# Kernel optimization log

Hardware: AMD Instinct MI355X
Metric: run time of the kernel (lower is better)

## Reference

```python
import jax, jax.numpy as jnp
import numpy as np

B, T, C = 4, 2048, 2048
H, HD = 16, 128  # n_heads, head_dim; C == H*HD


def _rope_rotate(x, cos, sin):
    """x: [b,t,h,d]; cos/sin: [t, d//2]. Complex multiply on interleaved pairs,
    matching torch view_as_complex on reshape(..., -1, 2)."""
    xr = x[..., 0::2]  # real parts  [b,t,h,d/2]
    xi = x[..., 1::2]  # imag parts
    c = cos[None, :, None, :]
    s = sin[None, :, None, :]
    or_ = xr * c - xi * s
    oi_ = xr * s + xi * c
    # interleave back: [..., d/2, 2] -> [..., d]
    return jnp.stack([or_, oi_], axis=-1).reshape(x.shape)


def setup_inputs() -> dict:
    key = jax.random.key(0)
    ks = jax.random.split(key, 6)
    x = jax.random.normal(ks[0], (B, T, C), dtype=jnp.float32)
    # causal boolean mask: True = attend
    attn_mask = jnp.tril(jnp.ones((T, T), dtype=bool))
    # standard RoPE frequencies (theta=10000)
    inv_freq = 1.0 / (10000.0 ** (np.arange(0, HD, 2, dtype=np.float32) / HD))
    ang = np.arange(T, dtype=np.float32)[:, None] * inv_freq[None, :]  # [T, HD/2]
    rope_cos = jnp.asarray(np.cos(ang))
    rope_sin = jnp.asarray(np.sin(ang))
    sc = 1.0 / np.sqrt(C)
    Wq = jax.random.normal(ks[1], (C, C), dtype=jnp.float32) * sc
    Wk = jax.random.normal(ks[2], (C, C), dtype=jnp.float32) * sc
    Wv = jax.random.normal(ks[3], (C, C), dtype=jnp.float32) * sc
    Wp = jax.random.normal(ks[4], (C, C), dtype=jnp.float32) * sc
    return {"x": x, "attn_mask": attn_mask, "rope_cos": rope_cos,
            "rope_sin": rope_sin, "Wq": Wq, "Wk": Wk, "Wv": Wv, "Wp": Wp}


def reference(x, attn_mask, rope_cos, rope_sin, Wq, Wk, Wv, Wp):
    b, t, c = x.shape
    # QKV projections (nn.Linear: y = x @ W.T), reshape to heads
    q = jnp.einsum('btc,dc->btd', x, Wq).reshape(b, t, H, HD)
    k = jnp.einsum('btc,dc->btd', x, Wk).reshape(b, t, H, HD)
    v = jnp.einsum('btc,dc->btd', x, Wv).reshape(b, t, H, HD)
    # RoPE on q, k
    q = _rope_rotate(q, rope_cos[:t], rope_sin[:t])
    k = _rope_rotate(k, rope_cos[:t], rope_sin[:t])
    # SDPA with boolean mask, scale 1/sqrt(head_dim)
    scores = jnp.einsum('bqhd,bkhd->bhqk', q, k) / jnp.sqrt(jnp.asarray(HD, x.dtype))
    neg = jnp.finfo(scores.dtype).min
    scores = jnp.where(attn_mask[None, None, :t, :t], scores, neg)
    attn = jax.nn.softmax(scores, axis=-1)
    out = jnp.einsum('bhqk,bkhd->bqhd', attn, v).reshape(b, t, H * HD)
    return jnp.einsum('btd,cd->btc', out, Wp)
```

## Files before the change

### kernel.cpp

```cpp
#include <hip/hip_runtime.h>

#define B_    4
#define T_    2048
#define C_    2048
#define H_    16
#define HD_   128
#define LDQK  4096

typedef __attribute__((ext_vector_type(8))) short short8v;
typedef __attribute__((ext_vector_type(4))) float float4v;
typedef __attribute__((ext_vector_type(16))) float float16v;

typedef const __attribute__((address_space(1))) void* gld_src_t;
typedef __attribute__((address_space(3))) void* gld_dst_t;
#define GLDS16(g, l) __builtin_amdgcn_global_load_lds((gld_src_t)(g), (gld_dst_t)(l), 16, 0, 0)

__device__ __forceinline__ unsigned short f2bf(float f) {
  unsigned int u = __float_as_uint(f);
  u += 0x7fffu + ((u >> 16) & 1u);
  return (unsigned short)(u >> 16);
}
__device__ __forceinline__ float bf2f(unsigned short s) {
  return __uint_as_float(((unsigned int)s) << 16);
}
__device__ __forceinline__ unsigned int cvtpk_bf16(float lo, float hi) {
  unsigned int r;
  asm("v_cvt_pk_bf16_f32 %0, %1, %2" : "=v"(r) : "v"(lo), "v"(hi));
  return r;
}

__global__ void cvt5_kernel(const float* __restrict__ x,
                            const float* __restrict__ wq, const float* __restrict__ wk,
                            const float* __restrict__ wv, const float* __restrict__ wp,
                            unsigned short* __restrict__ xbf, unsigned short* __restrict__ wdst) {
  int i = blockIdx.x * blockDim.x + threadIdx.x;
  const float4* s;
  ushort4* d;
  if (i < 4194304) {
    s = reinterpret_cast<const float4*>(x) + i;
    d = reinterpret_cast<ushort4*>(xbf) + i;
  } else {
    int j = i - 4194304;
    int w = j >> 20;
    const float* wsrc = (w == 0) ? wq : (w == 1) ? wk : (w == 2) ? wv : wp;
    s = reinterpret_cast<const float4*>(wsrc) + (j & 1048575);
    d = reinterpret_cast<ushort4*>(wdst) + j;
  }
  float4 v = *s;
  ushort4 o;
  o.x = f2bf(v.x); o.y = f2bf(v.y); o.z = f2bf(v.z); o.w = f2bf(v.w);
  *d = o;
}


#define ISSUE_HALF(MAT, HA, KT, CBUF)                                             \
  { const unsigned short* gp_ = (MAT) ? Bm : A;                                   \
    const size_t gb_ = (MAT) ? bbase : abase;                                     \
    _Pragma("unroll")                                                             \
    for (int i_ = 0; i_ < 2; ++i_) {                                              \
      int fo_ = (i_ * 512 + tid) * 16;                              \
      int rl_ = fo_ >> 7;                                            \
      int row_ = (HA) * 128 + rl_;                                                \
      int g_ = (fo_ >> 4) & 7;                                                    \
      int ce_ = ((g_ ^ (rl_ & 7)) << 3);              \
      GLDS16(gp_ + gb_ + (size_t)row_ * K + (KT) * 64 + ce_,                      \
             lds + (CBUF) * 65536 + (MAT) * 32768 + (HA) * 16384 + fo_);          \
    } }

#define RD_A(dst, MI, KK, CBUF)                                                   \
  { int row_ = wm * 128 + (MI) * 16 + lr;                                         \
    dst = *reinterpret_cast<const short8v*>(                                      \
        lds + (CBUF) * 65536 + row_ * 128 + (((KK) * 64 + lg * 16) ^ ((row_ & 7) << 4))); }

#define RD_B(dst, NI, KK, CBUF)                                                   \
  { int row_ = wn * 64 + (NI) * 16 + lr;                                          \
    dst = *reinterpret_cast<const short8v*>(                                      \
        lds + (CBUF) * 65536 + 32768 + row_ * 128 + (((KK) * 64 + lg * 16) ^ ((row_ & 7) << 4))); }

#define MFMA16(MB, AV, BV)                                                        \
    _Pragma("unroll")                                                             \
    for (int ni_ = 0; ni_ < 4; ++ni_) {                                           \
      _Pragma("unroll")                                                           \
      for (int mi_ = 0; mi_ < 4; ++mi_)                                           \
        acc[(MB)+mi_][ni_] = __builtin_amdgcn_mfma_f32_16x16x32_bf16(AV[mi_], BV[ni_], acc[(MB)+mi_][ni_], 0,0,0); \
    }

template<int MODE>
__global__ __launch_bounds__(512, 2)
void gemm256(const unsigned short* __restrict__ A, const unsigned short* __restrict__ Bm,
             void* __restrict__ Cout, unsigned short* __restrict__ vtp,
             int K, int NB, int ldc,
             const float* __restrict__ rc, const float* __restrict__ rs)
{
  extern __shared__ char lds[];
  const int tid = threadIdx.x;
  const int l = tid & 63, w = tid >> 6;
  const int lr = l & 15, lg = l >> 4;
  const int wm = w >> 2, wn = w & 3;

  const int nwg = (int)gridDim.x;
  const int orig = (int)blockIdx.x;
  const int qq = nwg >> 3, rr = nwg & 7;
  const int xcd = orig & 7, idx = orig >> 3;
  const int wg = (xcd < rr ? xcd * (qq + 1) : rr * (qq + 1) + (xcd - rr) * qq) + idx;
  const int bm = wg / NB, bn = wg % NB;

  const size_t abase = (size_t)bm * 256 * (size_t)K;
  const size_t bbase = (size_t)bn * 256 * (size_t)K;

  float4v acc[8][4];
  const float4v fz = {0.f, 0.f, 0.f, 0.f};
#pragma unroll
  for (int i = 0; i < 8; ++i)
#pragma unroll
    for (int j = 0; j < 4; ++j) acc[i][j] = fz;

  const int nk = K >> 6;

  ISSUE_HALF(1, 0, 0, 0)
  ISSUE_HALF(1, 1, 0, 0)
  ISSUE_HALF(0, 0, 0, 0)
  ISSUE_HALF(0, 1, 0, 0)
  asm volatile("s_waitcnt vmcnt(0)" ::: "memory");
  __builtin_amdgcn_s_barrier();

  short8v aC[4], aN[4], bC[4], bN[4];
  RD_A(aC[0], 0, 0, 0) RD_A(aC[1], 1, 0, 0) RD_A(aC[2], 2, 0, 0) RD_A(aC[3], 3, 0, 0)
  RD_B(bC[0], 0, 0, 0) RD_B(bC[1], 1, 0, 0) RD_B(bC[2], 2, 0, 0) RD_B(bC[3], 3, 0, 0)

  for (int t = 0; t < nk; ++t) {
    const int c = t & 1;

    if (t + 1 < nk) {
      ISSUE_HALF(1, 0, t + 1, c ^ 1)
      ISSUE_HALF(1, 1, t + 1, c ^ 1)
      ISSUE_HALF(0, 0, t + 1, c ^ 1)
      ISSUE_HALF(0, 1, t + 1, c ^ 1)
    }

    RD_A(aN[0], 4, 0, c) RD_A(aN[1], 5, 0, c) RD_A(aN[2], 6, 0, c) RD_A(aN[3], 7, 0, c)
    MFMA16(0, aC, bC)

    RD_A(aC[0], 0, 1, c) RD_A(aC[1], 1, 1, c) RD_A(aC[2], 2, 1, c) RD_A(aC[3], 3, 1, c)
    RD_B(bN[0], 0, 1, c) RD_B(bN[1], 1, 1, c) RD_B(bN[2], 2, 1, c) RD_B(bN[3], 3, 1, c)
    MFMA16(4, aN, bC)

    RD_A(aN[0], 4, 1, c) RD_A(aN[1], 5, 1, c) RD_A(aN[2], 6, 1, c) RD_A(aN[3], 7, 1, c)
    MFMA16(0, aC, bN)

    asm volatile("s_waitcnt lgkmcnt(0)" ::: "memory");
    __builtin_amdgcn_sched_barrier(0);
    asm volatile("s_waitcnt vmcnt(0)" ::: "memory");
    __builtin_amdgcn_s_barrier();

    MFMA16(4, aN, bN)

    if (t + 1 < nk) {
      RD_A(aC[0], 0, 0, c ^ 1) RD_A(aC[1], 1, 0, c ^ 1) RD_A(aC[2], 2, 0, c ^ 1) RD_A(aC[3], 3, 0, c ^ 1)
      RD_B(bC[0], 0, 0, c ^ 1) RD_B(bC[1], 1, 0, c ^ 1) RD_B(bC[2], 2, 0, c ^ 1) RD_B(bC[3], 3, 0, c ^ 1)
    }
  }

  const int row0 = bm * 256 + wm * 128;
  const int col0 = bn * 256 + wn * 64;
  if (MODE == 3 && bn >= 16) {
#pragma unroll
    for (int mi = 0; mi < 8; ++mi)
#pragma unroll
      for (int ni = 0; ni < 4; ++ni) {
        int vcol = col0 - 4096 + ni * 16 + lr;
        int hh = vcol >> 7, dd = vcol & 127;
        int row = row0 + mi * 16 + lg * 4;
        int bb = row >> 11, t0 = row & 2047;
        ushort4 o4;
        o4.x = f2bf(acc[mi][ni][0]); o4.y = f2bf(acc[mi][ni][1]);
        o4.z = f2bf(acc[mi][ni][2]); o4.w = f2bf(acc[mi][ni][3]);
        *reinterpret_cast<ushort4*>(vtp + (((size_t)(bb * 16 + hh)) << 18) + (((size_t)dd) << 11) + t0) = o4;
      }
  } else if (MODE == 3) {
    const float sgn = (lr & 1) ? 1.0f : -1.0f;
#pragma unroll
    for (int mi = 0; mi < 8; ++mi)
#pragma unroll
      for (int ni = 0; ni < 4; ++ni) {
        int col = col0 + ni * 16 + lr;
        int ii = (col & 127) >> 1;
#pragma unroll
        for (int r2 = 0; r2 < 4; ++r2) {
          int row = row0 + mi * 16 + lg * 4 + r2;
          int tt = row & 2047;
          float v = acc[mi][ni][r2];
          float vp = __shfl_xor(v, 1);
          float cs = rc[tt * 64 + ii];
          float sn = rs[tt * 64 + ii];
          float o = v * cs + sgn * vp * sn;
          ((unsigned short*)Cout)[(size_t)row * ldc + col] = f2bf(o);
        }
      }
  } else {
#pragma unroll
    for (int mi = 0; mi < 8; ++mi)
#pragma unroll
      for (int ni = 0; ni < 4; ++ni)
#pragma unroll
        for (int r2 = 0; r2 < 4; ++r2) {
          int row = row0 + mi * 16 + lg * 4 + r2;
          int col = col0 + ni * 16 + lr;
          ((float*)Cout)[(size_t)row * ldc + col] = acc[mi][ni][r2];
        }
  }
}

__global__ __launch_bounds__(256, 2)
void attn_kernel(const unsigned short* __restrict__ qk,
                 const unsigned short* __restrict__ vt,
                 unsigned short* __restrict__ out)
{
  __shared__ unsigned short Kl[2][64 * 128];
  __shared__ unsigned short Vl[2][128 * 64];

  const int wg = (int)blockIdx.x;
  const int bh = ((wg >> 6) << 3) | (wg & 7);
  const int bx = (wg >> 3) & 7;
  const int b = bh >> 4, h = bh & 15;
  const int tid = threadIdx.x, w = tid >> 6, l = tid & 63;
  const int q32 = l & 31, hi = l >> 5;
  const size_t rowbase = (size_t)b * T_;
  const unsigned short* kbase = qk + rowbase * LDQK + 2048 + h * HD_;
  const unsigned short* vbase = vt + (size_t)bh * (HD_ * (size_t)T_);
  const float SC = 0.12754089f;
  const float16v z16 = {0.f,0.f,0.f,0.f,0.f,0.f,0.f,0.f,0.f,0.f,0.f,0.f,0.f,0.f,0.f,0.f};

#define STAGE(kv0_, bi_)                                                          \
  {                                                                               \
    _Pragma("unroll")                                                             \
    for (int i_ = 0; i_ < 4; ++i_) {                                              \
      int fo = (i_ * 256 + tid) * 16;                                             \
      int row = fo >> 8;                                                          \
      int cb = (fo & 255) ^ ((row & 15) << 4);                                    \
      GLDS16(kbase + (size_t)((kv0_) + row) * LDQK + (cb >> 1), (char*)Kl[bi_] + fo); \
    }                                                                             \
    _Pragma("unroll")                                                             \
    for (int i_ = 0; i_ < 4; ++i_) {                                              \
      int fo = (i_ * 256 + tid) * 16;                                             \
      int r6 = (fo >> 8) & 63;                                                    \
      int s_ = (fo >> 7) & 1;                                                     \
      int dd = r6 | ((s_ ^ ((r6 >> 3) & 1)) << 6);                                \
      int k16 = ((fo >> 4) & 7) ^ (dd & 7);                                       \
      GLDS16(vbase + (size_t)dd * T_ + (kv0_) + k16 * 8, (char*)Vl[bi_] + fo);    \
    }                                                                             \
  }

  for (int sel = 0; sel < 2; ++sel) {
    const int qt = sel ? bx : (15 - bx);
    const int q0w = qt * 128 + w * 32;
    const int qg = q0w + q32;

    short8v qf[8];
#pragma unroll
    for (int kf = 0; kf < 8; ++kf) {
      short8v t = *reinterpret_cast<const short8v*>(
          qk + (rowbase + q0w + q32) * (size_t)LDQK + h * HD_ + kf * 16 + hi * 8);
      short8v r;
#pragma unroll
      for (int e = 0; e < 8; ++e) r[e] = (short)f2bf(bf2f((unsigned short)t[e]) * SC);
      qf[kf] = r;
    }

    float16v o[4];
#pragma unroll
    for (int db = 0; db < 4; ++db) o[db] = z16;
    float m_run = -1e30f, lsum = 0.f;

    const int nkv = 2 * (qt + 1);

    STAGE(0, 0);
    __syncthreads();

    for (int tile = 0; tile < nkv; ++tile) {
      const int kv0 = tile * 64;
      const int bi = tile & 1;
      if (tile + 1 < nkv) STAGE((tile + 1) * 64, bi ^ 1);

      if (kv0 <= q0w + 31) {
        float16v stv[2];
        stv[0] = z16; stv[1] = z16;
        __builtin_amdgcn_s_setprio(1);
#pragma unroll
        for (int kb = 0; kb < 2; ++kb) {
          int key = kb * 32 + q32;
          int swz = (key & 15) << 4;
          int rbase = key * 256;
#pragma unroll
          for (int kf = 0; kf < 8; ++kf) {
            short8v ak = *reinterpret_cast<const short8v*>(
                (char*)Kl[bi] + rbase + ((kf * 32 + hi * 16) ^ swz));
            stv[kb] = __builtin_amdgcn_mfma_f32_32x32x16_bf16(ak, qf[kf], stv[kb], 0, 0, 0);
          }
        }
        __builtin_amdgcn_s_setprio(0);
        if (kv0 + 63 > q0w) {
#pragma unroll
          for (int kb = 0; kb < 2; ++kb)
#pragma unroll
            for (int r = 0; r < 16; ++r) {
              int key = kv0 + kb * 32 + (r & 3) + 8 * ((r >> 2) & 3) + 4 * hi;
              if (key > qg) stv[kb][r] = -1e30f;
            }
        }
        float t16[16];
#pragma unroll
        for (int r = 0; r < 16; ++r) t16[r] = fmaxf(stv[0][r], stv[1][r]);
#pragma unroll
        for (int s = 8; s >= 1; s >>= 1)
#pragma unroll
          for (int r = 0; r < s; ++r) t16[r] = fmaxf(t16[r], t16[r + s]);
        float pm = fmaxf(t16[0], __shfl_xor(t16[0], 32));

        if (!__all(pm <= m_run + 8.0f)) {
          float mn = fmaxf(m_run, pm);
          float fac = exp2f(m_run - mn);
          lsum *= fac;
          m_run = mn;
#pragma unroll
          for (int r = 0; r < 16; ++r) {
            int src = (r & 3) + 8 * ((r >> 2) & 3) + 4 * hi;
            float fr = __shfl(fac, src);
#pragma unroll
            for (int db = 0; db < 4; ++db) o[db][r] *= fr;
          }
        }
        {
          float s16[16];
#pragma unroll
          for (int r = 0; r < 16; ++r) {
            float p0 = exp2f(stv[0][r] - m_run);
            float p1 = exp2f(stv[1][r] - m_run);
            stv[0][r] = p0; stv[1][r] = p1;
            s16[r] = p0 + p1;
          }
#pragma unroll
          for (int s = 8; s >= 1; s >>= 1)
#pragma unroll
            for (int r = 0; r < s; ++r) s16[r] += s16[r + s];
          lsum += s16[0] + __shfl_xor(s16[0], 32);
        }
        unsigned int pw0[8], pw1[8], xw0[8], xw1[8];
#pragma unroll
        for (int j = 0; j < 8; ++j) {
          pw0[j] = cvtpk_bf16(stv[0][2 * j], stv[0][2 * j + 1]);
          pw1[j] = cvtpk_bf16(stv[1][2 * j], stv[1][2 * j + 1]);
        }
#pragma unroll
        for (int j = 0; j < 8; ++j) {
          xw0[j] = __shfl_xor(pw0[j], 32);
          xw1[j] = __shfl_xor(pw1[j], 32);
        }
        union UW { unsigned int u[4]; short8v v; };
        short8v pb[4];
        {
          UW a0, a1, c0, c1;
          a0.u[0] = hi ? xw0[2] : pw0[0];  a0.u[1] = hi ? xw0[3] : pw0[1];
          a0.u[2] = hi ? pw0[2] : xw0[0];  a0.u[3] = hi ? pw0[3] : xw0[1];
          a1.u[0] = hi ? xw0[6] : pw0[4];  a1.u[1] = hi ? xw0[7] : pw0[5];
          a1.u[2] = hi ? pw0[6] : xw0[4];  a1.u[3] = hi ? pw0[7] : xw0[5];
          c0.u[0] = hi ? xw1[2] : pw1[0];  c0.u[1] = hi ? xw1[3] : pw1[1];
          c0.u[2] = hi ? pw1[2] : xw1[0];  c0.u[3] = hi ? pw1[3] : xw1[1];
          c1.u[0] = hi ? xw1[6] : pw1[4];  c1.u[1] = hi ? xw1[7] : pw1[5];
          c1.u[2] = hi ? pw1[6] : xw1[4];  c1.u[3] = hi ? pw1[7] : xw1[5];
          pb[0] = a0.v; pb[1] = a1.v; pb[2] = c0.v; pb[3] = c1.v;
        }
        __builtin_amdgcn_s_setprio(1);
#pragma unroll
        for (int db = 0; db < 4; ++db) {
          int dd = db * 32 + q32;
          int rb2 = (dd & 63) * 256 + ((((dd >> 6) ^ ((dd >> 3) & 1)) & 1) << 7);
          int swz = (dd & 7) << 4;
#pragma unroll
          for (int kb16 = 0; kb16 < 4; ++kb16) {
            short8v bv = *reinterpret_cast<const short8v*>(
                (char*)Vl[bi] + rb2 + ((kb16 * 32 + hi * 16) ^ swz));
            o[db] = __builtin_amdgcn_mfma_f32_32x32x16_bf16(pb[kb16], bv, o[db], 0, 0, 0);
          }
        }
        __builtin_amdgcn_s_setprio(0);
      }
      __syncthreads();
    }

    float linv = 1.0f / lsum;
#pragma unroll
    for (int r = 0; r < 16; ++r) {
      int src = (r & 3) + 8 * ((r >> 2) & 3) + 4 * hi;
      float lr_ = __shfl(linv, src);
      size_t rowoff = (rowbase + q0w + src) * (size_t)C_ + h * HD_ + q32;
#pragma unroll
      for (int db = 0; db < 4; ++db)
        out[rowoff + db * 32] = f2bf(o[db][r] * lr_);
    }
  }
#undef STAGE
}

extern "C" void kernel_launch(void* const* d_in, const int* in_sizes, int n_in,
                              void* d_out, int out_size, void* d_ws, size_t ws_size,
                              hipStream_t stream) {
  (void)in_sizes; (void)n_in; (void)out_size; (void)ws_size;
  const float* x  = (const float*)d_in[0];
  const float* rc = (const float*)d_in[2];
  const float* rs = (const float*)d_in[3];
  const float* Wq = (const float*)d_in[4];
  const float* Wk = (const float*)d_in[5];
  const float* Wv = (const float*)d_in[6];
  const float* Wp = (const float*)d_in[7];
  float* outp = (float*)d_out;

  unsigned short* ws    = (unsigned short*)d_ws;
  unsigned short* x_bf  = ws;
  unsigned short* wqkv  = x_bf + 16777216;
  unsigned short* wp_bf = wqkv + 12582912;
  unsigned short* qkbuf = wp_bf + 4194304;
  unsigned short* vtbuf = qkbuf + 33554432;
  unsigned short* ao    = x_bf;

  hipFuncSetAttribute((const void*)gemm256<0>, hipFuncAttributeMaxDynamicSharedMemorySize, 131072);
  hipFuncSetAttribute((const void*)gemm256<3>, hipFuncAttributeMaxDynamicSharedMemorySize, 131072);

  cvt5_kernel<<<32768, 256, 0, stream>>>(x, Wq, Wk, Wv, Wp, x_bf, wqkv);

  gemm256<3><<<dim3(768), 512, 131072, stream>>>(x_bf, wqkv, qkbuf, vtbuf, 2048, 24, 4096, rc, rs);

  attn_kernel<<<dim3(512), 256, 0, stream>>>(qkbuf, vtbuf, ao);

  gemm256<0><<<dim3(256), 512, 131072, stream>>>(ao, wp_bf, outp, nullptr, 2048, 8, 2048, nullptr, nullptr);
}
```

Measured before the change: 403.0 us.

## Load GEMM B operand directly from global into registers, bypassing LDS

```diff
diff --git a/kernel.cpp b/kernel.cpp
--- a/kernel.cpp
+++ b/kernel.cpp
@@ -53,29 +53,22 @@
 }
 
 
-#define ISSUE_HALF(MAT, HA, KT, CBUF)                                             \
-  { const unsigned short* gp_ = (MAT) ? Bm : A;                                   \
-    const size_t gb_ = (MAT) ? bbase : abase;                                     \
-    _Pragma("unroll")                                                             \
+#define ISSUE_A(HA, KT, CBUF)                                                     \
+  { _Pragma("unroll")                                                             \
     for (int i_ = 0; i_ < 2; ++i_) {                                              \
       int fo_ = (i_ * 512 + tid) * 16;                              \
       int rl_ = fo_ >> 7;                                            \
       int row_ = (HA) * 128 + rl_;                                                \
       int g_ = (fo_ >> 4) & 7;                                                    \
       int ce_ = ((g_ ^ (rl_ & 7)) << 3);              \
-      GLDS16(gp_ + gb_ + (size_t)row_ * K + (KT) * 64 + ce_,                      \
-             lds + (CBUF) * 65536 + (MAT) * 32768 + (HA) * 16384 + fo_);          \
+      GLDS16(A + abase + (size_t)row_ * K + (KT) * 64 + ce_,                      \
+             lds + (CBUF) * 32768 + (HA) * 16384 + fo_);                          \
     } }
 
 #define RD_A(dst, MI, KK, CBUF)                                                   \
   { int row_ = wm * 128 + (MI) * 16 + lr;                                         \
     dst = *reinterpret_cast<const short8v*>(                                      \
-        lds + (CBUF) * 65536 + row_ * 128 + (((KK) * 64 + lg * 16) ^ ((row_ & 7) << 4))); }
-
-#define RD_B(dst, NI, KK, CBUF)                                                   \
-  { int row_ = wn * 64 + (NI) * 16 + lr;                                          \
-    dst = *reinterpret_cast<const short8v*>(                                      \
-        lds + (CBUF) * 65536 + 32768 + row_ * 128 + (((KK) * 64 + lg * 16) ^ ((row_ & 7) << 4))); }
+        lds + (CBUF) * 32768 + row_ * 128 + (((KK) * 64 + lg * 16) ^ ((row_ & 7) << 4))); }
 
 #define MFMA16(MB, AV, BV)                                                        \
     _Pragma("unroll")                                                             \
@@ -106,7 +99,11 @@
   const int bm = wg / NB, bn = wg % NB;
 
   const size_t abase = (size_t)bm * 256 * (size_t)K;
-  const size_t bbase = (size_t)bn * 256 * (size_t)K;
+
+  const unsigned short* bptr[4];
+#pragma unroll
+  for (int ni = 0; ni < 4; ++ni)
+    bptr[ni] = Bm + (size_t)(bn * 256 + wn * 64 + ni * 16 + lr) * (size_t)K + lg * 8;
 
   float4v acc[8][4];
   const float4v fz = {0.f, 0.f, 0.f, 0.f};
@@ -117,33 +114,40 @@
 
   const int nk = K >> 6;
 
-  ISSUE_HALF(1, 0, 0, 0)
-  ISSUE_HALF(1, 1, 0, 0)
-  ISSUE_HALF(0, 0, 0, 0)
-  ISSUE_HALF(0, 1, 0, 0)
+  short8v aC[4], aN[4], bC[4], bN[4];
+
+  ISSUE_A(0, 0, 0)
+  ISSUE_A(1, 0, 0)
+#pragma unroll
+  for (int ni = 0; ni < 4; ++ni)
+    bC[ni] = *reinterpret_cast<const short8v*>(bptr[ni]);
   asm volatile("s_waitcnt vmcnt(0)" ::: "memory");
   __builtin_amdgcn_s_barrier();
 
-  short8v aC[4], aN[4], bC[4], bN[4];
   RD_A(aC[0], 0, 0, 0) RD_A(aC[1], 1, 0, 0) RD_A(aC[2], 2, 0, 0) RD_A(aC[3], 3, 0, 0)
-  RD_B(bC[0], 0, 0, 0) RD_B(bC[1], 1, 0, 0) RD_B(bC[2], 2, 0, 0) RD_B(bC[3], 3, 0, 0)
 
   for (int t = 0; t < nk; ++t) {
     const int c = t & 1;
 
+#pragma unroll
+    for (int ni = 0; ni < 4; ++ni)
+      bN[ni] = *reinterpret_cast<const short8v*>(bptr[ni] + t * 64 + 32);
     if (t + 1 < nk) {
-      ISSUE_HALF(1, 0, t + 1, c ^ 1)
-      ISSUE_HALF(1, 1, t + 1, c ^ 1)
-      ISSUE_HALF(0, 0, t + 1, c ^ 1)
-      ISSUE_HALF(0, 1, t + 1, c ^ 1)
+      ISSUE_A(0, t + 1, c ^ 1)
+      ISSUE_A(1, t + 1, c ^ 1)
     }
 
     RD_A(aN[0], 4, 0, c) RD_A(aN[1], 5, 0, c) RD_A(aN[2], 6, 0, c) RD_A(aN[3], 7, 0, c)
     MFMA16(0, aC, bC)
 
     RD_A(aC[0], 0, 1, c) RD_A(aC[1], 1, 1, c) RD_A(aC[2], 2, 1, c) RD_A(aC[3], 3, 1, c)
-    RD_B(bN[0], 0, 1, c) RD_B(bN[1], 1, 1, c) RD_B(bN[2], 2, 1, c) RD_B(bN[3], 3, 1, c)
     MFMA16(4, aN, bC)
+
+    if (t + 1 < nk) {
+#pragma unroll
+      for (int ni = 0; ni < 4; ++ni)
+        bC[ni] = *reinterpret_cast<const short8v*>(bptr[ni] + (t + 1) * 64);
+    }
 
     RD_A(aN[0], 4, 1, c) RD_A(aN[1], 5, 1, c) RD_A(aN[2], 6, 1, c) RD_A(aN[3], 7, 1, c)
     MFMA16(0, aC, bN)
@@ -157,7 +161,6 @@
 
     if (t + 1 < nk) {
       RD_A(aC[0], 0, 0, c ^ 1) RD_A(aC[1], 1, 0, c ^ 1) RD_A(aC[2], 2, 0, c ^ 1) RD_A(aC[3], 3, 0, c ^ 1)
-      RD_B(bC[0], 0, 0, c ^ 1) RD_B(bC[1], 1, 0, c ^ 1) RD_B(bC[2], 2, 0, c ^ 1) RD_B(bC[3], 3, 0, c ^ 1)
     }
   }
 
@@ -423,14 +426,14 @@
   unsigned short* vtbuf = qkbuf + 33554432;
   unsigned short* ao    = x_bf;
 
-  hipFuncSetAttribute((const void*)gemm256<0>, hipFuncAttributeMaxDynamicSharedMemorySize, 131072);
-  hipFuncSetAttribute((const void*)gemm256<3>, hipFuncAttributeMaxDynamicSharedMemorySize, 131072);
+  hipFuncSetAttribute((const void*)gemm256<0>, hipFuncAttributeMaxDynamicSharedMemorySize, 65536);
+  hipFuncSetAttribute((const void*)gemm256<3>, hipFuncAttributeMaxDynamicSharedMemorySize, 65536);
 
   cvt5_kernel<<<32768, 256, 0, stream>>>(x, Wq, Wk, Wv, Wp, x_bf, wqkv);
 
-  gemm256<3><<<dim3(768), 512, 131072, stream>>>(x_bf, wqkv, qkbuf, vtbuf, 2048, 24, 4096, rc, rs);
+  gemm256<3><<<dim3(768), 512, 65536, stream>>>(x_bf, wqkv, qkbuf, vtbuf, 2048, 24, 4096, rc, rs);
 
   attn_kernel<<<dim3(512), 256, 0, stream>>>(qkbuf, vtbuf, ao);
 
-  gemm256<0><<<dim3(256), 512, 131072, stream>>>(ao, wp_bf, outp, nullptr, 2048, 8, 2048, nullptr, nullptr);
-}
+  gemm256<0><<<dim3(256), 512, 65536, stream>>>(ao, wp_bf, outp, nullptr, 2048, 8, 2048, nullptr, nullptr);
+}
```

Result: slower. 562.3 us (+39.5%).
